# Performance work log

Hardware: AMD Instinct MI355X
Metric: run time of the kernel (lower is better)

Reference implementation:

```python
import jax, jax.numpy as jnp
import numpy as np
import math

B, S, E, H = 2, 2048, 1024, 16
HD = E // H          # head_dim = 64
HX = 64              # helix_dim
P = HX // 2          # helix pairs = 32

def setup_inputs() -> dict:
    key = jax.random.key(0)
    ks = jax.random.split(key, 12)
    sc = 0.02
    return {
        "x":    jax.random.normal(ks[0], (B, S, E), dtype=jnp.float32),
        "Wq":   jax.random.normal(ks[1], (E, E), dtype=jnp.float32) * sc,
        "bq":   jnp.zeros((E,), dtype=jnp.float32),
        "Wk":   jax.random.normal(ks[2], (E, E), dtype=jnp.float32) * sc,
        "bk":   jnp.zeros((E,), dtype=jnp.float32),
        "Wv":   jax.random.normal(ks[3], (E, E), dtype=jnp.float32) * sc,
        "bv":   jnp.zeros((E,), dtype=jnp.float32),
        "Wo":   jax.random.normal(ks[4], (E, E), dtype=jnp.float32) * sc,
        "bo":   jnp.zeros((E,), dtype=jnp.float32),
        "Whel": jax.random.normal(ks[5], (H, HX, HD), dtype=jnp.float32) * sc,
        "bhel": jnp.zeros((H, HX), dtype=jnp.float32),
    }

def _l2norm(x, eps=1e-12):
    # torch F.normalize(p=2, dim=-1): x / max(||x||, eps)
    n = jnp.sqrt(jnp.sum(x * x, axis=-1, keepdims=True))
    return x / jnp.maximum(n, eps)

def _scramble(t):
    # faithful to torch: (B,S,2) -> transpose(1,2) -> reshape(B,S,2),
    # vectorized over (H,P): t is (B,H,P,S,2)
    b, h, p, s, _ = t.shape
    return jnp.swapaxes(t, -1, -2).reshape(b, h, p, s, 2)

def reference(x, Wq, bq, Wk, bk, Wv, bv, Wo, bo, Whel, bhel):
    b, s, e = x.shape
    h, hx, hd = Whel.shape
    p = hx // 2
    q = x @ Wq.T + bq
    k = x @ Wk.T + bk
    v = x @ Wv.T + bv
    qh = q.reshape(b, s, h, hd)
    kh = k.reshape(b, s, h, hd)
    # per-head helical projections: (B,S,H,HX)
    q_hel = jnp.einsum('bshd,hed->bshe', qh, Whel) + bhel
    k_hel = jnp.einsum('bshd,hed->bshe', kh, Whel) + bhel
    # split into 2D coords, normalize each pair: (B,H,P,S,2)
    qn = _l2norm(q_hel.reshape(b, s, h, p, 2)).transpose(0, 2, 3, 1, 4)
    kn = _l2norm(k_hel.reshape(b, s, h, p, 2)).transpose(0, 2, 3, 1, 4)
    qn = _scramble(qn)
    kn = _scramble(kn)
    # helical similarity averaged over pairs: (B,H,S,S)
    helical = jnp.einsum('bhpsc,bhptc->bhst', qn, kn) / p
    # standard scaled dot-product scores
    dot = jnp.einsum('bshd,bthd->bhst', qh, kh) / math.sqrt(hd)
    alpha = 0.5
    attn = jax.nn.softmax(alpha * dot + (1.0 - alpha) * helical, axis=-1)
    vh = v.reshape(b, s, h, hd)
    out = jnp.einsum('bhst,bthd->bshd', attn, vh).reshape(b, s, e)
    return out @ Wo.T + bo
```

## Files before the change

### kernel.cpp

```cpp
#include <hip/hip_runtime.h>
#include <hip/hip_bf16.h>


typedef unsigned short u16;
typedef unsigned int u32;
typedef __attribute__((ext_vector_type(8))) __bf16 bf16x8;
typedef __attribute__((ext_vector_type(4))) float f32x4;
typedef __attribute__((ext_vector_type(16))) float f32x16;

union BFrag { u32 u[4]; bf16x8 b; };

__device__ __forceinline__ u16 f2b(float f) {
  u32 u = __float_as_uint(f);
  u32 r = (u + 0x7fffu + ((u >> 16) & 1u)) >> 16;
  return (u16)r;
}
__device__ __forceinline__ float b2f(u16 h) {
  return __uint_as_float(((u32)h) << 16);
}

__device__ __forceinline__ f32x4 mfma16(bf16x8 a, bf16x8 b, f32x4 c) {
  return __builtin_amdgcn_mfma_f32_16x16x32_bf16(a, b, c, 0, 0, 0);
}
__device__ __forceinline__ f32x16 mfma32(bf16x8 a, bf16x8 b, f32x16 c) {
  return __builtin_amdgcn_mfma_f32_32x32x16_bf16(a, b, c, 0, 0, 0);
}

__device__ __forceinline__ void gld16(void* lds, const void* g) {
  __builtin_amdgcn_global_load_lds(
      (const __attribute__((address_space(1))) unsigned int*)g,
      (__attribute__((address_space(3))) unsigned int*)lds, 16, 0, 0);
}

__device__ __forceinline__ void pl32swap(u32& a, u32& b, int l5) {
#if __has_builtin(__builtin_amdgcn_permlane32_swap)
  typedef unsigned int u32x2v __attribute__((ext_vector_type(2)));
  u32x2v r = __builtin_amdgcn_permlane32_swap(a, b, false, false);
  a = r[0];
  b = r[1];
#else
  u32 ea = __shfl_xor((int)a, 32);
  u32 eb = __shfl_xor((int)b, 32);
  u32 na = l5 ? eb : a;
  u32 nb = l5 ? b : ea;
  a = na;
  b = nb;
#endif
}

#define LOG2E 1.4426950408889634f

#define PIPE_BARRIER(N)                                         \
  do {                                                          \
    __builtin_amdgcn_sched_barrier(0);                          \
    asm volatile("s_waitcnt vmcnt(" #N ")" ::: "memory");       \
    __builtin_amdgcn_s_barrier();                               \
    __builtin_amdgcn_sched_barrier(0);                          \
  } while (0)

__global__ __launch_bounds__(256) void cast_kernel(
    const float* __restrict__ x,  const float* __restrict__ wq,
    const float* __restrict__ wk, const float* __restrict__ wv,
    const float* __restrict__ wo, const float* __restrict__ whel,
    u16* __restrict__ xb, u16* __restrict__ wb, u16* __restrict__ wob,
    u16* __restrict__ whb) {
  long long q = (long long)blockIdx.x * 256 + threadIdx.x;
  const float* s; u16* d; long long base;
  if (q < 1048576)      { s = x;    d = xb;            base = 0; }
  else if (q < 1310720) { s = wq;   d = wb;            base = 1048576; }
  else if (q < 1572864) { s = wk;   d = wb + 1048576;  base = 1310720; }
  else if (q < 1835008) { s = wv;   d = wb + 2097152;  base = 1572864; }
  else if (q < 2097152) { s = wo;   d = wob;           base = 1835008; }
  else                  { s = whel; d = whb;           base = 2097152; }
  long long e = (q - base) * 4;
  float4 v = *(const float4*)(s + e);
  ushort4 o;
  o.x = f2b(v.x); o.y = f2b(v.y); o.z = f2b(v.z); o.w = f2b(v.w);
  *(ushort4*)(d + e) = o;
}

__global__ __launch_bounds__(256, 3) void qkv_gemm(
    const u16* __restrict__ xb, const u16* __restrict__ wb,
    const float* __restrict__ bq, const float* __restrict__ bk,
    const float* __restrict__ bv, const u16* __restrict__ whb,
    const float* __restrict__ bhel,
    u16* __restrict__ Qcat, u16* __restrict__ Kcat, u16* __restrict__ vt) {
  union SM {
    struct { u16 Al[3][128][32]; u16 Bl[3][128][32]; } m;
    struct { u16 T[64][136]; } t;
    struct { u16 Th[4][32][72]; u16 Hs[2][128][64]; } e;
  };
  __shared__ SM sm;
  const int nt = blockIdx.x, mt = blockIdx.y;
  const int which = nt >> 3;
  const int n0 = (nt & 7) << 7;
  const int m0 = mt << 7;
  const int tid = threadIdx.x;
  const int wave = tid >> 6, lane = tid & 63;
  const int g = lane >> 4, c15 = lane & 15;
  const int wm = wave & 1, wn = wave >> 1;
  const u16* Wp = wb + (long long)which * (1024 * 1024) + n0 * 1024;
  const u16* Ap = xb + m0 * 1024;
  const int srow = tid >> 2;
  const int scol = (lane & 3) << 3;

  f32x4 acc[4][4];
#pragma unroll
  for (int i = 0; i < 4; i++)
#pragma unroll
    for (int j = 0; j < 4; j++) acc[i][j] = f32x4{0.f, 0.f, 0.f, 0.f};

  gld16(&sm.m.Al[0][srow][scol],      Ap + srow * 1024 + scol);
  gld16(&sm.m.Al[0][64 + srow][scol], Ap + (64 + srow) * 1024 + scol);
  gld16(&sm.m.Bl[0][srow][scol],      Wp + srow * 1024 + scol);
  gld16(&sm.m.Bl[0][64 + srow][scol], Wp + (64 + srow) * 1024 + scol);
  gld16(&sm.m.Al[1][srow][scol],      Ap + srow * 1024 + 32 + scol);
  gld16(&sm.m.Al[1][64 + srow][scol], Ap + (64 + srow) * 1024 + 32 + scol);
  gld16(&sm.m.Bl[1][srow][scol],      Wp + srow * 1024 + 32 + scol);
  gld16(&sm.m.Bl[1][64 + srow][scol], Wp + (64 + srow) * 1024 + 32 + scol);

  int cur = 0;
  for (int it = 0; it < 32; ++it) {
    if (it < 31) { PIPE_BARRIER(4); } else { PIPE_BARRIER(0); }
    if (it + 2 < 32) {
      const int pf = (cur >= 1) ? cur - 1 : 2;
      const int kn = (it + 2) << 5;
      gld16(&sm.m.Al[pf][srow][scol],      Ap + srow * 1024 + kn + scol);
      gld16(&sm.m.Al[pf][64 + srow][scol],
            Ap + (64 + srow) * 1024 + kn + scol);
      gld16(&sm.m.Bl[pf][srow][scol],      Wp + srow * 1024 + kn + scol);
      gld16(&sm.m.Bl[pf][64 + srow][scol],
            Wp + (64 + srow) * 1024 + kn + scol);
    }
    bf16x8 a[4], b[4];
#pragma unroll
    for (int i = 0; i < 4; i++)
      a[i] = *(const bf16x8*)&sm.m.Al[cur][wm * 64 + i * 16 + c15][g * 8];
#pragma unroll
    for (int j = 0; j < 4; j++)
      b[j] = *(const bf16x8*)&sm.m.Bl[cur][wn * 64 + j * 16 + c15][g * 8];
#pragma unroll
    for (int i = 0; i < 4; i++)
#pragma unroll
      for (int j = 0; j < 4; j++) acc[i][j] = mfma16(a[i], b[j], acc[i][j]);
    cur = (cur == 2) ? 0 : cur + 1;
  }

  if (which == 2) {
#pragma unroll
    for (int half = 0; half < 2; ++half) {
      __syncthreads();
      if (wn == half) {
#pragma unroll
        for (int i = 0; i < 4; i++)
#pragma unroll
          for (int j = 0; j < 4; j++)
#pragma unroll
            for (int r = 0; r < 4; r++) {
              int nloc = j * 16 + c15;
              int mloc = wm * 64 + i * 16 + g * 4 + r;
              float v = acc[i][j][r] + bv[n0 + half * 64 + nloc];
              sm.t.T[nloc][mloc] = f2b(v);
            }
      }
      __syncthreads();
#pragma unroll
      for (int it = 0; it < 4; ++it) {
        int idx = it * 256 + tid;
        int row = idx >> 4;
        int cm = (idx & 15) * 8;
        int col = n0 + half * 64 + row;
        int hh = col >> 6, dd = col & 63;
        int m = m0 + cm;
        int bb2 = m >> 11, s = m & 2047;
        *(uint4*)&vt[(((bb2 * 16 + hh) * 64) + dd) * 2048 + s] =
            *(const uint4*)&sm.t.T[row][cm];
      }
    }
    return;
  }

  const float* bias = (which == 0) ? bq : bk;
  const float fold = (which == 0) ? (0.0625f * LOG2E) : 1.0f;
  const float osc  = (which == 0) ? (0.125f * LOG2E) : 0.125f;
  const int h0 = n0 >> 6;
  const int hsel = h0 + wn;
  u16* Dst = ((which == 0) ? Qcat : Kcat);

  bf16x8 wf[2][4];
#pragma unroll
  for (int kh = 0; kh < 2; ++kh)
#pragma unroll
    for (int nf = 0; nf < 4; ++nf)
      wf[kh][nf] = *(const bf16x8*)(whb + hsel * 4096 + (nf * 16 + c15) * 64 +
                                    kh * 32 + g * 8);

  __syncthreads();
  const int bb2 = m0 >> 11;
  const int ubase = (m0 & 2047) >> 1;

#pragma unroll
  for (int half = 0; half < 2; ++half) {
#pragma unroll
    for (int i2 = 0; i2 < 2; ++i2) {
      int i = half * 2 + i2;
#pragma unroll
      for (int j = 0; j < 4; ++j)
#pragma unroll
        for (int r = 0; r < 4; ++r) {
          int row = m0 + wm * 64 + i * 16 + g * 4 + r;
          int col = n0 + wn * 64 + j * 16 + c15;
          float vraw = acc[i][j][r] + bias[col];
          int bb = row >> 11, s = row & 2047;
          int d = col & 63;
          Dst[(((long long)(bb * 16 + hsel) * 2048) + s) * 128 + d] =
              f2b(vraw * fold);
          sm.e.Th[wave][i2 * 16 + g * 4 + r][j * 16 + c15] = f2b(vraw);
        }
    }
    f32x4 hacc[2][4];
#pragma unroll
    for (int mf = 0; mf < 2; ++mf)
#pragma unroll
      for (int nf = 0; nf < 4; ++nf) hacc[mf][nf] = f32x4{0.f, 0.f, 0.f, 0.f};
#pragma unroll
    for (int kh = 0; kh < 2; ++kh) {
      bf16x8 a0 = *(const bf16x8*)&sm.e.Th[wave][c15][kh * 32 + g * 8];
      bf16x8 a1 = *(const bf16x8*)&sm.e.Th[wave][16 + c15][kh * 32 + g * 8];
#pragma unroll
      for (int nf = 0; nf < 4; ++nf) {
        hacc[0][nf] = mfma16(a0, wf[kh][nf], hacc[0][nf]);
        hacc[1][nf] = mfma16(a1, wf[kh][nf], hacc[1][nf]);
      }
    }
#pragma unroll
    for (int mf = 0; mf < 2; ++mf)
#pragma unroll
      for (int nf = 0; nf < 4; ++nf)
#pragma unroll
        for (int r = 0; r < 4; ++r) {
          int e = nf * 16 + c15;
          float v = hacc[mf][nf][r] + bhel[hsel * 64 + e];
          float pp = __shfl_xor(v, 1);
          float nn = sqrtf(v * v + pp * pp);
          float o = v / fmaxf(nn, 1e-12f) * osc;
          int tl = wm * 64 + half * 32 + mf * 16 + g * 4 + r;
          sm.e.Hs[wn][(e & 1) * 64 + (tl >> 1)][(e & ~1) | (tl & 1)] = f2b(o);
        }
  }
  __syncthreads();
#pragma unroll
  for (int it = 0; it < 8; ++it) {
    int idx = it * 256 + tid;
    int hh = idx >> 10;
    int hr = (idx >> 3) & 127;
    int ck = idx & 7;
    int coord = hr >> 6, ul = hr & 63;
    int row_out = coord * 1024 + ubase + ul;
    *(uint4*)&Dst[(((long long)(bb2 * 16 + h0 + hh) * 2048) + row_out) * 128 +
                  64 + ck * 8] = *(const uint4*)&sm.e.Hs[hh][hr][ck * 8];
  }
}

__global__ __launch_bounds__(512, 4) void attn_kernel(
    const u16* __restrict__ Qcat, const u16* __restrict__ Kcat,
    const u16* __restrict__ vt, u16* __restrict__ AO) {
  __shared__ u16 Kl[3][64][128];
  __shared__ u16 Vl[3][64][64];
  __shared__ float denl[2][128];
  const int bh = blockIdx.x, qt = blockIdx.y;
  const int bb = bh >> 4, h = bh & 15;
  const int q0 = qt << 7;
  const int tid = threadIdx.x;
  const int w = tid >> 6, lane = tid & 63;
  const int wq = w & 3, wt = w >> 2;
  const int l31 = lane & 31, l5 = lane >> 5;
  const u16* Qb = Qcat + (long long)bh * (2048 * 128);
  const u16* Kb = Kcat + (long long)bh * (2048 * 128);
  const u16* Vb = vt + (long long)bh * (64 * 2048);

  bf16x8 qf[8];
  {
    const u16* qrow = Qb + (q0 + 32 * wq + l31) * 128 + l5 * 8;
#pragma unroll
    for (int ks = 0; ks < 8; ++ks) qf[ks] = *(const bf16x8*)(qrow + ks * 16);
  }

  const int ll = tid;
  const int krow0 = ll >> 4;
  const int kp = ll & 15;
  const int ksrc0 = (kp & 8) | ((kp & 7) ^ (krow0 & 7));
  const int krow1 = 32 + krow0;
  const int ksrc1 = (kp & 8) | ((kp & 7) ^ (krow1 & 7));
  const int vd = ll >> 3;
  const int vsrc = (ll & 7) ^ (vd & 7);

  gld16(((u16*)Kl[0]) + ll * 8,        Kb + krow0 * 128 + ksrc0 * 8);
  gld16(((u16*)Kl[0]) + 4096 + ll * 8, Kb + krow1 * 128 + ksrc1 * 8);
  gld16(((u16*)Vl[0]) + ll * 8,        Vb + vd * 2048 + vsrc * 8);
  gld16(((u16*)Kl[1]) + ll * 8,        Kb + (64 + krow0) * 128 + ksrc0 * 8);
  gld16(((u16*)Kl[1]) + 4096 + ll * 8, Kb + (64 + krow1) * 128 + ksrc1 * 8);
  gld16(((u16*)Vl[1]) + ll * 8,        Vb + vd * 2048 + 64 + vsrc * 8);

  f32x16 accO0, accO1;
#pragma unroll
  for (int i = 0; i < 16; ++i) { accO0[i] = 0.f; accO1[i] = 0.f; }
  float den = 0.f;

  const int krow = 32 * wt + l31;
  const int kr7 = krow & 7;

  int cur = 0;
  for (int t = 0; t < 32; ++t) {
    if (t < 31) { PIPE_BARRIER(3); } else { PIPE_BARRIER(0); }
    if (t + 2 < 32) {
      const int pf = (cur >= 1) ? cur - 1 : 2;
      const int t2 = (t + 2) << 6;
      u16* Kd = (u16*)Kl[pf];
      gld16(Kd + ll * 8,        Kb + (t2 + krow0) * 128 + ksrc0 * 8);
      gld16(Kd + 4096 + ll * 8, Kb + (t2 + krow1) * 128 + ksrc1 * 8);
      gld16(((u16*)Vl[pf]) + ll * 8, Vb + vd * 2048 + t2 + vsrc * 8);
    }

    f32x16 accS;
#pragma unroll
    for (int i = 0; i < 16; ++i) accS[i] = 0.f;
#pragma unroll
    for (int ks = 0; ks < 8; ++ks) {
      int lc = 2 * ks + l5;
      int p = (lc & 8) | ((lc & 7) ^ kr7);
      bf16x8 ak = *(const bf16x8*)&Kl[cur][krow][p * 8];
      accS = mfma32(ak, qf[ks], accS);
    }

    u32 D0[2], D1[2], D2[2], D3[2];
#pragma unroll
    for (int rr = 0; rr < 4; ++rr) {
      float p0 = __builtin_amdgcn_exp2f(accS[4 * rr + 0]);
      float p1 = __builtin_amdgcn_exp2f(accS[4 * rr + 1]);
      float p2 = __builtin_amdgcn_exp2f(accS[4 * rr + 2]);
      float p3 = __builtin_amdgcn_exp2f(accS[4 * rr + 3]);
      den += (p0 + p1) + (p2 + p3);
      u32 lo = __builtin_amdgcn_perm(__float_as_uint(p1), __float_as_uint(p0),
                                     0x07060302u);
      u32 hi = __builtin_amdgcn_perm(__float_as_uint(p3), __float_as_uint(p2),
                                     0x07060302u);
      if (rr == 0) { D0[0] = lo; D0[1] = hi; }
      else if (rr == 1) { D1[0] = lo; D1[1] = hi; }
      else if (rr == 2) { D2[0] = lo; D2[1] = hi; }
      else { D3[0] = lo; D3[1] = hi; }
    }
    BFrag A0, A1;
    A0.u[0] = D0[0]; A0.u[2] = D1[0]; pl32swap(A0.u[0], A0.u[2], l5);
    A0.u[1] = D0[1]; A0.u[3] = D1[1]; pl32swap(A0.u[1], A0.u[3], l5);
    A1.u[0] = D2[0]; A1.u[2] = D3[0]; pl32swap(A1.u[0], A1.u[2], l5);
    A1.u[1] = D2[1]; A1.u[3] = D3[1]; pl32swap(A1.u[1], A1.u[3], l5);

#pragma unroll
    for (int dq = 0; dq < 2; ++dq) {
      int d = 32 * dq + l31;
      int d7 = d & 7;
#pragma unroll
      for (int ks = 0; ks < 2; ++ks) {
        int lc = 4 * wt + 2 * ks + l5;
        bf16x8 bvf = *(const bf16x8*)&Vl[cur][d][((lc ^ d7) & 7) * 8];
        if (dq == 0) accO0 = mfma32(ks ? A1.b : A0.b, bvf, accO0);
        else         accO1 = mfma32(ks ? A1.b : A0.b, bvf, accO1);
      }
    }
    cur = (cur == 2) ? 0 : cur + 1;
  }

  den += __shfl_xor(den, 32);
  if (lane < 32) denl[wt][32 * wq + lane] = den;
  __syncthreads();

  float* S = (float*)Kl;
  if (wt == 1) {
#pragma unroll
    for (int r = 0; r < 16; ++r) {
      int qr = (r & 3) + 8 * (r >> 2) + 4 * l5;
      S[(wq * 32 + qr) * 64 + l31] = accO0[r];
      S[(wq * 32 + qr) * 64 + 32 + l31] = accO1[r];
    }
  }
  __syncthreads();
  if (wt == 0) {
#pragma unroll
    for (int r = 0; r < 16; ++r) {
      int qr = (r & 3) + 8 * (r >> 2) + 4 * l5;
      int ql = 32 * wq + qr;
      float inv = 1.0f / (denl[0][ql] + denl[1][ql]);
      float o0 = (accO0[r] + S[(wq * 32 + qr) * 64 + l31]) * inv;
      float o1 = (accO1[r] + S[(wq * 32 + qr) * 64 + 32 + l31]) * inv;
      long long base = ((long long)(bb * 2048 + q0 + ql) * 1024) + h * 64;
      AO[base + l31] = f2b(o0);
      AO[base + 32 + l31] = f2b(o1);
    }
  }
}

__global__ __launch_bounds__(256, 2) void out_gemm(
    const u16* __restrict__ AO, const u16* __restrict__ wob,
    const float* __restrict__ bo, float* __restrict__ out) {
  __shared__ u16 Al[3][128][32];
  __shared__ u16 Bl[3][64][32];
  const int n0 = blockIdx.x << 6;
  const int m0 = blockIdx.y << 7;
  const int tid = threadIdx.x;
  const int wave = tid >> 6, lane = tid & 63;
  const int g = lane >> 4, c15 = lane & 15;
  const int wm = wave & 1, wn = wave >> 1;
  const u16* Wp = wob + n0 * 1024;
  const u16* Ap = AO + m0 * 1024;
  const int srow = tid >> 2;
  const int scol = (tid & 3) << 3;

  f32x4 acc[4][2];
#pragma unroll
  for (int i = 0; i < 4; i++)
#pragma unroll
    for (int j = 0; j < 2; j++) acc[i][j] = f32x4{0.f, 0.f, 0.f, 0.f};

  gld16(&Al[0][srow][scol],      Ap + srow * 1024 + scol);
  gld16(&Al[0][64 + srow][scol], Ap + (64 + srow) * 1024 + scol);
  gld16(&Bl[0][srow][scol],      Wp + srow * 1024 + scol);
  gld16(&Al[1][srow][scol],      Ap + srow * 1024 + 32 + scol);
  gld16(&Al[1][64 + srow][scol], Ap + (64 + srow) * 1024 + 32 + scol);
  gld16(&Bl[1][srow][scol],      Wp + srow * 1024 + 32 + scol);

  int cur = 0;
  for (int it = 0; it < 32; ++it) {
    if (it < 31) { PIPE_BARRIER(3); } else { PIPE_BARRIER(0); }
    if (it + 2 < 32) {
      const int pf = (cur >= 1) ? cur - 1 : 2;
      const int kn = (it + 2) << 5;
      gld16(&Al[pf][srow][scol],      Ap + srow * 1024 + kn + scol);
      gld16(&Al[pf][64 + srow][scol], Ap + (64 + srow) * 1024 + kn + scol);
      gld16(&Bl[pf][srow][scol],      Wp + srow * 1024 + kn + scol);
    }
    bf16x8 a[4], b[2];
#pragma unroll
    for (int i = 0; i < 4; i++)
      a[i] = *(const bf16x8*)&Al[cur][wm * 64 + i * 16 + c15][g * 8];
#pragma unroll
    for (int j = 0; j < 2; j++)
      b[j] = *(const bf16x8*)&Bl[cur][wn * 32 + j * 16 + c15][g * 8];
#pragma unroll
    for (int i = 0; i < 4; i++)
#pragma unroll
      for (int j = 0; j < 2; j++) acc[i][j] = mfma16(a[i], b[j], acc[i][j]);
    cur = (cur == 2) ? 0 : cur + 1;
  }
#pragma unroll
  for (int i = 0; i < 4; i++)
#pragma unroll
    for (int j = 0; j < 2; j++)
#pragma unroll
      for (int r = 0; r < 4; r++) {
        int row = m0 + wm * 64 + i * 16 + g * 4 + r;
        int col = n0 + wn * 32 + j * 16 + c15;
        out[row * 1024 + col] = acc[i][j][r] + bo[col];
      }
}

extern "C" void kernel_launch(void* const* d_in, const int* in_sizes, int n_in,
                              void* d_out, int out_size, void* d_ws,
                              size_t ws_size, hipStream_t stream) {
  const float* x    = (const float*)d_in[0];
  const float* Wq   = (const float*)d_in[1];
  const float* bq   = (const float*)d_in[2];
  const float* Wk   = (const float*)d_in[3];
  const float* bk   = (const float*)d_in[4];
  const float* Wv   = (const float*)d_in[5];
  const float* bv   = (const float*)d_in[6];
  const float* Wo   = (const float*)d_in[7];
  const float* bo   = (const float*)d_in[8];
  const float* Whel = (const float*)d_in[9];
  const float* bhel = (const float*)d_in[10];
  float* out = (float*)d_out;

  char* ws = (char*)d_ws;
  u16* xb   = (u16*)(ws + 0);
  u16* wb   = (u16*)(ws + 8388608);
  u16* wob  = (u16*)(ws + 14680064);
  u16* whb  = (u16*)(ws + 16777216);
  u16* Qcat = (u16*)(ws + 16908288);
  u16* Kcat = (u16*)(ws + 33685504);
  u16* vt   = (u16*)(ws + 50462720);
  u16* AO   = (u16*)(ws + 58851328);

  cast_kernel<<<dim3(8256), dim3(256), 0, stream>>>(x, Wq, Wk, Wv, Wo, Whel,
                                                    xb, wb, wob, whb);
  qkv_gemm<<<dim3(24, 32), dim3(256), 0, stream>>>(xb, wb, bq, bk, bv, whb,
                                                   bhel, Qcat, Kcat, vt);
  attn_kernel<<<dim3(32, 16), dim3(512), 0, stream>>>(Qcat, Kcat, vt, AO);
  out_gemm<<<dim3(16, 32), dim3(256), 0, stream>>>(AO, wob, bo, out);
}
```

Baseline: 219.4 us.

## Split QKV GEMM tile across 8 waves instead of 4

The qkv_gemm block grows from 256 to 512 threads, so each wave computes a 64x32 sub-tile rather than 64x64, with one load per thread per stage instead of two. The helical epilogue is rearranged so waves share per-head staging tiles and each wave computes 16 rows of the helix projection, with extra __syncthreads between phases. The aim is more resident waves to hide latency and fewer accumulator registers per thread. The cost is more barriers, duplicated A-fragment LDS reads across the N-split waves, and helix weight fragments reloaded inside the half loop.

```diff
diff --git a/kernel.cpp b/kernel.cpp
--- a/kernel.cpp
+++ b/kernel.cpp
@@ -79,7 +79,7 @@
   *(ushort4*)(d + e) = o;
 }
 
-__global__ __launch_bounds__(256, 3) void qkv_gemm(
+__global__ __launch_bounds__(512, 6) void qkv_gemm(
     const u16* __restrict__ xb, const u16* __restrict__ wb,
     const float* __restrict__ bq, const float* __restrict__ bk,
     const float* __restrict__ bv, const u16* __restrict__ whb,
@@ -96,53 +96,46 @@
   const int n0 = (nt & 7) << 7;
   const int m0 = mt << 7;
   const int tid = threadIdx.x;
-  const int wave = tid >> 6, lane = tid & 63;
+  const int w = tid >> 6, lane = tid & 63;
   const int g = lane >> 4, c15 = lane & 15;
-  const int wm = wave & 1, wn = wave >> 1;
+  const int wm = w & 1, hl = (w >> 1) & 1, ch = w >> 2;
+  const int nbase = hl * 64 + ch * 32;
   const u16* Wp = wb + (long long)which * (1024 * 1024) + n0 * 1024;
   const u16* Ap = xb + m0 * 1024;
   const int srow = tid >> 2;
-  const int scol = (lane & 3) << 3;
-
-  f32x4 acc[4][4];
+  const int scol = (tid & 3) << 3;
+
+  f32x4 acc[4][2];
 #pragma unroll
   for (int i = 0; i < 4; i++)
 #pragma unroll
-    for (int j = 0; j < 4; j++) acc[i][j] = f32x4{0.f, 0.f, 0.f, 0.f};
-
-  gld16(&sm.m.Al[0][srow][scol],      Ap + srow * 1024 + scol);
-  gld16(&sm.m.Al[0][64 + srow][scol], Ap + (64 + srow) * 1024 + scol);
-  gld16(&sm.m.Bl[0][srow][scol],      Wp + srow * 1024 + scol);
-  gld16(&sm.m.Bl[0][64 + srow][scol], Wp + (64 + srow) * 1024 + scol);
-  gld16(&sm.m.Al[1][srow][scol],      Ap + srow * 1024 + 32 + scol);
-  gld16(&sm.m.Al[1][64 + srow][scol], Ap + (64 + srow) * 1024 + 32 + scol);
-  gld16(&sm.m.Bl[1][srow][scol],      Wp + srow * 1024 + 32 + scol);
-  gld16(&sm.m.Bl[1][64 + srow][scol], Wp + (64 + srow) * 1024 + 32 + scol);
+    for (int j = 0; j < 2; j++) acc[i][j] = f32x4{0.f, 0.f, 0.f, 0.f};
+
+  gld16(&sm.m.Al[0][srow][scol], Ap + srow * 1024 + scol);
+  gld16(&sm.m.Bl[0][srow][scol], Wp + srow * 1024 + scol);
+  gld16(&sm.m.Al[1][srow][scol], Ap + srow * 1024 + 32 + scol);
+  gld16(&sm.m.Bl[1][srow][scol], Wp + srow * 1024 + 32 + scol);
 
   int cur = 0;
   for (int it = 0; it < 32; ++it) {
-    if (it < 31) { PIPE_BARRIER(4); } else { PIPE_BARRIER(0); }
+    if (it < 31) { PIPE_BARRIER(2); } else { PIPE_BARRIER(0); }
     if (it + 2 < 32) {
       const int pf = (cur >= 1) ? cur - 1 : 2;
       const int kn = (it + 2) << 5;
-      gld16(&sm.m.Al[pf][srow][scol],      Ap + srow * 1024 + kn + scol);
-      gld16(&sm.m.Al[pf][64 + srow][scol],
-            Ap + (64 + srow) * 1024 + kn + scol);
-      gld16(&sm.m.Bl[pf][srow][scol],      Wp + srow * 1024 + kn + scol);
-      gld16(&sm.m.Bl[pf][64 + srow][scol],
-            Wp + (64 + srow) * 1024 + kn + scol);
-    }
-    bf16x8 a[4], b[4];
+      gld16(&sm.m.Al[pf][srow][scol], Ap + srow * 1024 + kn + scol);
+      gld16(&sm.m.Bl[pf][srow][scol], Wp + srow * 1024 + kn + scol);
+    }
+    bf16x8 a[4], b[2];
 #pragma unroll
     for (int i = 0; i < 4; i++)
       a[i] = *(const bf16x8*)&sm.m.Al[cur][wm * 64 + i * 16 + c15][g * 8];
 #pragma unroll
-    for (int j = 0; j < 4; j++)
-      b[j] = *(const bf16x8*)&sm.m.Bl[cur][wn * 64 + j * 16 + c15][g * 8];
+    for (int j = 0; j < 2; j++)
+      b[j] = *(const bf16x8*)&sm.m.Bl[cur][nbase + j * 16 + c15][g * 8];
 #pragma unroll
     for (int i = 0; i < 4; i++)
 #pragma unroll
-      for (int j = 0; j < 4; j++) acc[i][j] = mfma16(a[i], b[j], acc[i][j]);
+      for (int j = 0; j < 2; j++) acc[i][j] = mfma16(a[i], b[j], acc[i][j]);
     cur = (cur == 2) ? 0 : cur + 1;
   }
 
@@ -150,14 +143,14 @@
 #pragma unroll
     for (int half = 0; half < 2; ++half) {
       __syncthreads();
-      if (wn == half) {
+      if (hl == half) {
 #pragma unroll
         for (int i = 0; i < 4; i++)
 #pragma unroll
-          for (int j = 0; j < 4; j++)
+          for (int j = 0; j < 2; j++)
 #pragma unroll
             for (int r = 0; r < 4; r++) {
-              int nloc = j * 16 + c15;
+              int nloc = ch * 32 + j * 16 + c15;
               int mloc = wm * 64 + i * 16 + g * 4 + r;
               float v = acc[i][j][r] + bv[n0 + half * 64 + nloc];
               sm.t.T[nloc][mloc] = f2b(v);
@@ -165,8 +158,8 @@
       }
       __syncthreads();
 #pragma unroll
-      for (int it = 0; it < 4; ++it) {
-        int idx = it * 256 + tid;
+      for (int it = 0; it < 2; ++it) {
+        int idx = it * 512 + tid;
         int row = idx >> 4;
         int cm = (idx & 15) * 8;
         int col = n0 + half * 64 + row;
@@ -184,16 +177,9 @@
   const float fold = (which == 0) ? (0.0625f * LOG2E) : 1.0f;
   const float osc  = (which == 0) ? (0.125f * LOG2E) : 0.125f;
   const int h0 = n0 >> 6;
-  const int hsel = h0 + wn;
+  const int hsel = h0 + hl;
+  const int pid = hl * 2 + wm;
   u16* Dst = ((which == 0) ? Qcat : Kcat);
-
-  bf16x8 wf[2][4];
-#pragma unroll
-  for (int kh = 0; kh < 2; ++kh)
-#pragma unroll
-    for (int nf = 0; nf < 4; ++nf)
-      wf[kh][nf] = *(const bf16x8*)(whb + hsel * 4096 + (nf * 16 + c15) * 64 +
-                                    kh * 32 + g * 8);
 
   __syncthreads();
   const int bb2 = m0 >> 11;
@@ -205,53 +191,56 @@
     for (int i2 = 0; i2 < 2; ++i2) {
       int i = half * 2 + i2;
 #pragma unroll
-      for (int j = 0; j < 4; ++j)
+      for (int j = 0; j < 2; ++j)
 #pragma unroll
         for (int r = 0; r < 4; ++r) {
           int row = m0 + wm * 64 + i * 16 + g * 4 + r;
-          int col = n0 + wn * 64 + j * 16 + c15;
+          int d = ch * 32 + j * 16 + c15;
+          int col = n0 + hl * 64 + d;
           float vraw = acc[i][j][r] + bias[col];
           int bb = row >> 11, s = row & 2047;
-          int d = col & 63;
           Dst[(((long long)(bb * 16 + hsel) * 2048) + s) * 128 + d] =
               f2b(vraw * fold);
-          sm.e.Th[wave][i2 * 16 + g * 4 + r][j * 16 + c15] = f2b(vraw);
+          sm.e.Th[pid][i2 * 16 + g * 4 + r][d] = f2b(vraw);
         }
     }
-    f32x4 hacc[2][4];
-#pragma unroll
-    for (int mf = 0; mf < 2; ++mf)
-#pragma unroll
-      for (int nf = 0; nf < 4; ++nf) hacc[mf][nf] = f32x4{0.f, 0.f, 0.f, 0.f};
+    __syncthreads();
+
+    bf16x8 wf[2][4];
+#pragma unroll
+    for (int kh = 0; kh < 2; ++kh)
+#pragma unroll
+      for (int nf = 0; nf < 4; ++nf)
+        wf[kh][nf] = *(const bf16x8*)(whb + hsel * 4096 +
+                                      (nf * 16 + c15) * 64 + kh * 32 + g * 8);
+
+    f32x4 hacc[4];
+#pragma unroll
+    for (int nf = 0; nf < 4; ++nf) hacc[nf] = f32x4{0.f, 0.f, 0.f, 0.f};
 #pragma unroll
     for (int kh = 0; kh < 2; ++kh) {
-      bf16x8 a0 = *(const bf16x8*)&sm.e.Th[wave][c15][kh * 32 + g * 8];
-      bf16x8 a1 = *(const bf16x8*)&sm.e.Th[wave][16 + c15][kh * 32 + g * 8];
-#pragma unroll
-      for (int nf = 0; nf < 4; ++nf) {
-        hacc[0][nf] = mfma16(a0, wf[kh][nf], hacc[0][nf]);
-        hacc[1][nf] = mfma16(a1, wf[kh][nf], hacc[1][nf]);
+      bf16x8 a0 = *(const bf16x8*)&sm.e.Th[pid][ch * 16 + c15][kh * 32 + g * 8];
+#pragma unroll
+      for (int nf = 0; nf < 4; ++nf)
+        hacc[nf] = mfma16(a0, wf[kh][nf], hacc[nf]);
+    }
+#pragma unroll
+    for (int nf = 0; nf < 4; ++nf)
+#pragma unroll
+      for (int r = 0; r < 4; ++r) {
+        int e = nf * 16 + c15;
+        float v = hacc[nf][r] + bhel[hsel * 64 + e];
+        float pp = __shfl_xor(v, 1);
+        float nn = sqrtf(v * v + pp * pp);
+        float o = v / fmaxf(nn, 1e-12f) * osc;
+        int tl = wm * 64 + half * 32 + ch * 16 + g * 4 + r;
+        sm.e.Hs[hl][(e & 1) * 64 + (tl >> 1)][(e & ~1) | (tl & 1)] = f2b(o);
       }
-    }
-#pragma unroll
-    for (int mf = 0; mf < 2; ++mf)
-#pragma unroll
-      for (int nf = 0; nf < 4; ++nf)
-#pragma unroll
-        for (int r = 0; r < 4; ++r) {
-          int e = nf * 16 + c15;
-          float v = hacc[mf][nf][r] + bhel[hsel * 64 + e];
-          float pp = __shfl_xor(v, 1);
-          float nn = sqrtf(v * v + pp * pp);
-          float o = v / fmaxf(nn, 1e-12f) * osc;
-          int tl = wm * 64 + half * 32 + mf * 16 + g * 4 + r;
-          sm.e.Hs[wn][(e & 1) * 64 + (tl >> 1)][(e & ~1) | (tl & 1)] = f2b(o);
-        }
-  }
-  __syncthreads();
-#pragma unroll
-  for (int it = 0; it < 8; ++it) {
-    int idx = it * 256 + tid;
+    __syncthreads();
+  }
+#pragma unroll
+  for (int it = 0; it < 4; ++it) {
+    int idx = it * 512 + tid;
     int hh = idx >> 10;
     int hr = (idx >> 3) & 127;
     int ck = idx & 7;
@@ -492,7 +481,7 @@
 
   cast_kernel<<<dim3(8256), dim3(256), 0, stream>>>(x, Wq, Wk, Wv, Wo, Whel,
                                                     xb, wb, wob, whb);
-  qkv_gemm<<<dim3(24, 32), dim3(256), 0, stream>>>(xb, wb, bq, bk, bv, whb,
+  qkv_gemm<<<dim3(24, 32), dim3(512), 0, stream>>>(xb, wb, bq, bk, bv, whb,
                                                    bhel, Qcat, Kcat, vt);
   attn_kernel<<<dim3(32, 16), dim3(512), 0, stream>>>(Qcat, Kcat, vt, AO);
   out_gemm<<<dim3(16, 32), dim3(256), 0, stream>>>(AO, wob, bo, out);
```

New measurement: 224.3 us. 2.2% more time.
